# Performance work log

Measured on AMD Instinct MI355X. Metric: run time of the kernel, lower is better.

The kernel has to match this reference:

```python
import jax, jax.numpy as jnp
import numpy as np

B = 4096
ED = 128          # EMBEDDING_DIM
HD = 64           # HIDDEN_DIM
LH = 128          # LSTM_HIDDEN_DIM
IN_DIM = ED * (12 + 48 + 1)  # 7808
N_ABILITY, N_MOVE = 300, 900


def setup_inputs() -> dict:
    key = jax.random.key(0)
    ks = jax.random.split(key, 16)
    s = lambda k, shape, scale=0.05: (jax.random.normal(k, shape, dtype=jnp.float32) * scale)
    return {
        "ability_ids": jax.random.randint(ks[0], (B, 12), 0, N_ABILITY),
        "move_ids": jax.random.randint(ks[1], (B, 48), 0, N_MOVE),
        "numerical": s(ks[2], (B, 84), 1.0),
        "mask": (jax.random.uniform(ks[3], (B, 9)) > 0.3).astype(jnp.float32),
        "h0": jnp.zeros((B, LH), jnp.float32),
        "c0": jnp.zeros((B, LH), jnp.float32),
        "ability_emb": s(ks[4], (N_ABILITY, ED), 1.0),
        "move_emb": s(ks[5], (N_MOVE, ED), 1.0),
        "num_W": s(ks[6], (ED, 84)),
        "num_b": s(ks[7], (ED,)),
        "Wih": s(ks[8], (4 * LH, IN_DIM), 0.01),
        "Whh": s(ks[9], (4 * LH, LH)),
        "bih": s(ks[10], (4 * LH,)),
        "bhh": s(ks[11], (4 * LH,)),
        "W1": s(ks[12], (HD, LH)),
        "b1": s(ks[13], (HD,)),
        "W2": s(ks[14], (ED, HD)),
        "b2": s(ks[15], (ED,)),
        "Wa": s(jax.random.fold_in(key, 100), (9, ED)),
        "ba": s(jax.random.fold_in(key, 101), (9,)),
    }


def reference(ability_ids, move_ids, numerical, mask, h0, c0,
              ability_emb, move_emb, num_W, num_b,
              Wih, Whh, bih, bhh, W1, b1, W2, b2, Wa, ba):
    # Gather + concat: [B, 12*ED] + [B, 48*ED] + [B, ED] -> [B, 7808]
    ab = ability_emb[ability_ids].reshape(ability_ids.shape[0], 12 * ED)
    mv = move_emb[move_ids].reshape(move_ids.shape[0], 48 * ED)
    num = numerical @ num_W.T + num_b
    x = jnp.concatenate([ab, mv, num], axis=-1)

    # Single-timestep LSTM (torch gate order: i, f, g, o)
    gates = x @ Wih.T + bih + h0 @ Whh.T + bhh
    i, f, g, o = jnp.split(gates, 4, axis=-1)
    i, f, o = jax.nn.sigmoid(i), jax.nn.sigmoid(f), jax.nn.sigmoid(o)
    g = jnp.tanh(g)
    c1 = f * c0 + i * g
    h1 = o * jnp.tanh(c1)

    # MLP head + action logits
    feat = jax.nn.relu(h1 @ W1.T + b1) @ W2.T + b2
    probs = jax.nn.softmax(feat @ Wa.T + ba, axis=-1)

    # Masked renormalization; fall back to unmasked probs when mask kills everything
    masked = probs * mask
    ssum = masked.sum(-1, keepdims=True)
    out = jnp.where(ssum > 0, masked / jnp.where(ssum > 0, ssum, 1.0), probs)
    return out, h1, c1
```

## Files before the change

kernel.cpp:

```cpp
#include <hip/hip_runtime.h>
#include <hip/hip_bf16.h>
#include <stdint.h>
#include <stddef.h>

typedef __bf16 bf16;
typedef __bf16 bf16x4 __attribute__((ext_vector_type(4)));
typedef __bf16 bf16x8 __attribute__((ext_vector_type(8)));
typedef float f32x4 __attribute__((ext_vector_type(4)));

#define BATCH 4096
#define KIH 7808
#define KTOT 7936
#define NG 512
#define LH 128
#define HD 64
#define ED 128
#define SPLITK 4

#define OFF_WCAT 0u
#define OFF_GPART 8126464u
#define OFF_XT   24903680u
#define OFF_AB   27000832u
#define OFF_MV   27077632u
#define OFF_ADDR 27308032u
#define OFF_W1F  29405184u
#define OFF_W2F  29421568u
#define OFF_WAF  29437952u
#define OFF_NB   29442048u

#define O_H1 (BATCH * 9)
#define O_C1 (BATCH * 9 + BATCH * LH)

#define PREP_BP 2048
#define PREP_CW (PREP_BP + 512)
#define PREP_CE (PREP_CW + 150)
#define PREP_TOT (PREP_CE + 1)

typedef const __attribute__((address_space(1))) uint32_t* gas_ptr;
typedef __attribute__((address_space(3))) uint32_t* las_ptr;

__device__ __forceinline__ void async16(const void* g, void* l) {
    __builtin_amdgcn_global_load_lds((gas_ptr)g, (las_ptr)l, 16, 0, 0);
}

__global__ void prep(const int* __restrict__ ab_ids,
                     const int* __restrict__ mv_ids,
                     const float* __restrict__ numerical,
                     const float* __restrict__ h0,
                     const float* __restrict__ numW,
                     const float* __restrict__ numb,
                     const float* __restrict__ Wih,
                     const float* __restrict__ Whh,
                     const float* __restrict__ ab_emb,
                     const float* __restrict__ mv_emb,
                     const float* __restrict__ W1,
                     const float* __restrict__ W2,
                     const float* __restrict__ Wa,
                     uint8_t* __restrict__ ws) {
    const int bid = blockIdx.x;
    const int t = threadIdx.x;

    if (bid < PREP_BP) {
        bf16* xtail = (bf16*)(ws + OFF_XT);
        uint32_t* addrs = (uint32_t*)(ws + OFF_ADDR);
        const int h = t >> 7;
        const int th = t & 127;
        const int b = bid * 2 + h;

        __shared__ int ids[2][60];
        if (th < 60)
            ids[h][th] = (th < 12) ? ab_ids[b * 12 + th]
                                   : mv_ids[b * 48 + (th - 12)];

        const float v = (th < 84) ? numerical[(size_t)b * 84 + th] : 0.f;
        xtail[(size_t)b * 256 + th] = (bf16)v;
        xtail[(size_t)b * 256 + 128 + th] = (bf16)h0[(size_t)b * LH + th];
        __syncthreads();

        if (th < 64) {
            uint32_t off;
            if (th < 12) off = OFF_AB + (uint32_t)ids[h][th] * 256u;
            else if (th < 60) off = OFF_MV + (uint32_t)ids[h][th] * 256u;
            else if (th == 60) off = OFF_XT + (uint32_t)b * 512u;
            else if (th == 61) off = OFF_XT + (uint32_t)b * 512u + 256u;
            else off = OFF_XT;
            addrs[(size_t)b * 64 + th] = off;
        }
    } else if (bid < PREP_CW) {
        bf16* Wcat = (bf16*)(ws + OFF_WCAT);
        float* nbias = (float*)(ws + OFF_NB);
        const int n = bid - PREP_BP;

        __shared__ float wrow[128];
        __shared__ float nbs[128];
        if (t < 128) wrow[t] = Wih[(size_t)n * KIH + 7680 + t];
        else nbs[t - 128] = numb[t - 128];
        __syncthreads();

        const float* src_ih = Wih + (size_t)n * KIH;
        bf16* dst = Wcat + (size_t)n * KTOT;
        for (int k4 = t; k4 < 1920; k4 += 256) {
            const int k = k4 * 4;
            const float4 v = *(const float4*)(src_ih + k);
            bf16x4 o = {(bf16)v.x, (bf16)v.y, (bf16)v.z, (bf16)v.w};
            *(bf16x4*)(dst + k) = o;
        }
        if (t < 84) {
            float acc = 0.f;
#pragma unroll 4
            for (int e = 0; e < 128; ++e)
                acc += wrow[e] * numW[e * 84 + t];
            dst[7680 + t] = (bf16)acc;
        } else if (t < 128) {
            dst[7680 + t] = (bf16)0.f;
        } else {
            const int tt = t - 128;
            dst[KIH + tt] = (bf16)Whh[(size_t)n * LH + tt];
        }
        if (t == 255) {
            float a = 0.f;
#pragma unroll 4
            for (int e = 0; e < 128; ++e) a += wrow[e] * nbs[e];
            nbias[n] = a;
        }
    } else if (bid < PREP_CE) {
        bf16* ab8 = (bf16*)(ws + OFF_AB);
        bf16* mv8 = (bf16*)(ws + OFF_MV);
        const int i = ((bid - PREP_CW) * 256 + t) * 4;
        const bool isab = i < 300 * 128;
        const float4 v = isab ? *(const float4*)(ab_emb + i)
                              : *(const float4*)(mv_emb + (i - 300 * 128));
        bf16x4 o = {(bf16)v.x, (bf16)v.y, (bf16)v.z, (bf16)v.w};
        if (isab) *(bf16x4*)(ab8 + i) = o;
        else *(bf16x4*)(mv8 + (i - 300 * 128)) = o;
    } else {
        bf16* W1f = (bf16*)(ws + OFF_W1F);
        bf16* W2f = (bf16*)(ws + OFF_W2F);
        bf16* Waf = (bf16*)(ws + OFF_WAF);
        for (int e = t; e < 8192; e += 256) {
            const int j = e & 7, ln = (e >> 3) & 63, fid = e >> 9;
            const int kt = fid & 3, nt = fid >> 2;
            const int n = nt * 16 + (ln & 15);
            const int k = kt * 32 + (ln >> 4) * 8 + j;
            W1f[e] = (bf16)W1[n * 128 + k];
        }
        for (int e = t; e < 8192; e += 256) {
            const int j = e & 7, ln = (e >> 3) & 63, fid = e >> 9;
            const int kt = fid & 1, nt = fid >> 1;
            const int n = nt * 16 + (ln & 15);
            const int k = kt * 32 + (ln >> 4) * 8 + j;
            W2f[e] = (bf16)W2[n * 64 + k];
        }
        for (int e = t; e < 2048; e += 256) {
            const int j = e & 7, ln = (e >> 3) & 63, kt = e >> 9;
            const int n = ln & 15;
            const int k = kt * 32 + (ln >> 4) * 8 + j;
            Waf[e] = (n < 9) ? (bf16)Wa[n * 128 + k] : (bf16)0.f;
        }
    }
}

__global__ __launch_bounds__(256, 3) void gemm_gates(
    const uint8_t* __restrict__ wsbase,
    const bf16* __restrict__ Wcat,
    const uint32_t* __restrict__ addrs,
    bf16* __restrict__ gpart) {
    __shared__ bf16 As[2][64 * 64];
    __shared__ bf16 Bs[2][128 * 64];
    __shared__ uint32_t adr[17][64];

    const int tid = threadIdx.x;
    const int w = tid >> 6;
    const int lane = tid & 63;
    const int bm = blockIdx.x;
    const int bn = blockIdx.y;
    const int bz = blockIdx.z;
    const int kt_beg = bz * 31;
    const int kt_end = kt_beg + 31;

    const int s0 = kt_beg >> 1;
    const int ns = ((kt_end - 1) >> 1) - s0 + 1;
    for (int i = tid; i < ns * 64; i += 256) {
        adr[i >> 6][i & 63] =
            addrs[(size_t)(bm * 64 + (i & 63)) * 64 + s0 + (i >> 6)];
    }

    const int r_l = lane >> 3;
    const int sc16 = ((lane & 7) ^ r_l) * 16;

    const int wn = w & 1;
    const int wk = w >> 1;
    const int n0 = wn * 64;
    const int kk8 = wk * 4 + (lane >> 4);
    const int fl = lane & 15;

    f32x4 acc[4][4];
#pragma unroll
    for (int i = 0; i < 4; ++i)
#pragma unroll
        for (int j = 0; j < 4; ++j)
#pragma unroll
            for (int r = 0; r < 4; ++r) acc[i][j][r] = 0.f;

    __syncthreads();

    auto stage = [&](int kt, int pb) {
        const int k0 = kt * 64;
        const int sl = (kt >> 1) - s0;
        const int hb = (kt & 1) * 128;
#pragma unroll
        for (int j = 0; j < 2; ++j) {
            const int row = (w * 2 + j) * 8 + r_l;
            const uint8_t* gsrc = wsbase + adr[sl][row] + hb + sc16;
            async16(gsrc, (void*)&As[pb][((w * 2 + j) * 64 + lane) * 8]);
        }
#pragma unroll
        for (int j = 0; j < 4; ++j) {
            const int row = (w * 4 + j) * 8 + r_l;
            const bf16* gsrc = Wcat + (size_t)(bn * 128 + row) * KTOT + k0 + (sc16 >> 1);
            async16(gsrc, (void*)&Bs[pb][((w * 4 + j) * 64 + lane) * 8]);
        }
    };

    stage(kt_beg, 0);

    for (int kt = kt_beg; kt < kt_end; ++kt) {
        const int pb = (kt - kt_beg) & 1;
        __syncthreads();
        if (kt + 1 < kt_end) stage(kt + 1, pb ^ 1);

        const bf16* Ab = &As[pb][0];
        const bf16* Bb = &Bs[pb][0];

        bf16x8 bfr[4];
#pragma unroll
        for (int tj = 0; tj < 4; ++tj) {
            const int n = n0 + tj * 16 + fl;
            bfr[tj] = *(const bf16x8*)&Bb[n * 64 + ((kk8 ^ (n & 7)) * 8)];
        }
#pragma unroll
        for (int ti = 0; ti < 4; ++ti) {
            const int m = ti * 16 + fl;
            const bf16x8 af = *(const bf16x8*)&Ab[m * 64 + ((kk8 ^ (m & 7)) * 8)];
#pragma unroll
            for (int tj = 0; tj < 4; ++tj)
                acc[ti][tj] = __builtin_amdgcn_mfma_f32_16x16x32_bf16(
                    af, bfr[tj], acc[ti][tj], 0, 0, 0);
        }
    }

    __syncthreads();
    float* red = (wn == 0) ? (float*)&As[0][0] : (float*)&Bs[0][0];
    if (wk == 1) {
#pragma unroll
        for (int ti = 0; ti < 4; ++ti)
#pragma unroll
            for (int tj = 0; tj < 4; ++tj)
#pragma unroll
                for (int r = 0; r < 4; ++r)
                    red[((ti * 4 + tj) * 4 + r) * 64 + lane] = acc[ti][tj][r];
    }
    __syncthreads();

    if (wk == 0) {
        bf16* gdst = gpart + (size_t)bz * BATCH * NG;
        const int mlo = (lane >> 4) * 4;
#pragma unroll
        for (int ti = 0; ti < 4; ++ti)
#pragma unroll
            for (int tj = 0; tj < 4; ++tj) {
                const int mg = bm * 64 + ti * 16 + mlo;
                const int ng = bn * 128 + n0 + tj * 16 + fl;
                bf16* dst = gdst + (size_t)mg * NG + ng;
#pragma unroll
                for (int r = 0; r < 4; ++r)
                    dst[(size_t)r * NG] = (bf16)(
                        acc[ti][tj][r] + red[((ti * 4 + tj) * 4 + r) * 64 + lane]);
            }
    }
}

__global__ __launch_bounds__(256) void tail(
    const bf16* __restrict__ gpart,
    const float* __restrict__ bih, const float* __restrict__ bhh,
    const float* __restrict__ nbias, const float* __restrict__ c0,
    const float* __restrict__ mask,
    const bf16* __restrict__ W1f, const bf16* __restrict__ W2f,
    const bf16* __restrict__ Waf,
    const float* __restrict__ b1, const float* __restrict__ b2,
    const float* __restrict__ ba,
    float* __restrict__ out) {
    __shared__ bf16 hS[16 * 128];
    __shared__ bf16 uS[16 * 64];
    __shared__ bf16 fS[16 * 128];

    const int t = threadIdx.x;
    const int bid = blockIdx.x;
    const int b0 = bid * 16;

    {
        const int r = t >> 4;
        const int uc = (t & 15) * 8;
        const int b = b0 + r;

        float gv[4][8];
#pragma unroll
        for (int q = 0; q < 4; ++q)
#pragma unroll
            for (int hh = 0; hh < 2; ++hh) {
                const f32x4 va = *(const f32x4*)(bih + q * 128 + uc + hh * 4);
                const f32x4 vb = *(const f32x4*)(bhh + q * 128 + uc + hh * 4);
                const f32x4 vn = *(const f32x4*)(nbias + q * 128 + uc + hh * 4);
#pragma unroll
                for (int j = 0; j < 4; ++j)
                    gv[q][hh * 4 + j] = va[j] + vb[j] + vn[j];
            }
#pragma unroll
        for (int z = 0; z < SPLITK; ++z) {
            const bf16* gz = gpart + ((size_t)z * BATCH + b) * NG;
#pragma unroll
            for (int q = 0; q < 4; ++q) {
                const bf16x8 v = *(const bf16x8*)(gz + q * 128 + uc);
#pragma unroll
                for (int j = 0; j < 8; ++j) gv[q][j] += (float)v[j];
            }
        }

        const f32x4 c0a = *(const f32x4*)(c0 + (size_t)b * LH + uc);
        const f32x4 c0b = *(const f32x4*)(c0 + (size_t)b * LH + uc + 4);
        float h1v[8], c1v[8];
        bf16x8 hv8;
#pragma unroll
        for (int j = 0; j < 8; ++j) {
            const float iv = 1.f / (1.f + __expf(-gv[0][j]));
            const float fv = 1.f / (1.f + __expf(-gv[1][j]));
            const float gg = tanhf(gv[2][j]);
            const float ov = 1.f / (1.f + __expf(-gv[3][j]));
            const float c0j = (j < 4) ? c0a[j] : c0b[j - 4];
            const float c1 = fv * c0j + iv * gg;
            const float h1 = ov * tanhf(c1);
            c1v[j] = c1;
            h1v[j] = h1;
            hv8[j] = (bf16)h1;
        }
        *(bf16x8*)&hS[r * 128 + uc] = hv8;
        *(f32x4*)(out + O_H1 + (size_t)b * LH + uc) = *(const f32x4*)&h1v[0];
        *(f32x4*)(out + O_H1 + (size_t)b * LH + uc + 4) = *(const f32x4*)&h1v[4];
        *(f32x4*)(out + O_C1 + (size_t)b * LH + uc) = *(const f32x4*)&c1v[0];
        *(f32x4*)(out + O_C1 + (size_t)b * LH + uc + 4) = *(const f32x4*)&c1v[4];
    }
    __syncthreads();

    const int nl = t & 15, kg = (t & 63) >> 4;

    if (t < 64) {
        bf16x8 ah[4];
#pragma unroll
        for (int kt = 0; kt < 4; ++kt)
            ah[kt] = *(const bf16x8*)&hS[nl * 128 + kt * 32 + kg * 8];
#pragma unroll
        for (int nt = 0; nt < 4; ++nt) {
            f32x4 a = {0.f, 0.f, 0.f, 0.f};
#pragma unroll
            for (int kt = 0; kt < 4; ++kt)
                a = __builtin_amdgcn_mfma_f32_16x16x32_bf16(
                    ah[kt], *(const bf16x8*)&W1f[((nt * 4 + kt) * 64 + t) * 8],
                    a, 0, 0, 0);
            const int n = nt * 16 + nl;
            const float bb = b1[n];
#pragma unroll
            for (int rr = 0; rr < 4; ++rr)
                uS[(kg * 4 + rr) * 64 + n] = (bf16)fmaxf(a[rr] + bb, 0.f);
        }
    }
    __syncthreads();

    if (t < 64) {
        bf16x8 au[2];
#pragma unroll
        for (int kt = 0; kt < 2; ++kt)
            au[kt] = *(const bf16x8*)&uS[nl * 64 + kt * 32 + kg * 8];
#pragma unroll
        for (int nt = 0; nt < 8; ++nt) {
            f32x4 a = {0.f, 0.f, 0.f, 0.f};
#pragma unroll
            for (int kt = 0; kt < 2; ++kt)
                a = __builtin_amdgcn_mfma_f32_16x16x32_bf16(
                    au[kt], *(const bf16x8*)&W2f[((nt * 2 + kt) * 64 + t) * 8],
                    a, 0, 0, 0);
            const int n = nt * 16 + nl;
            const float bb = b2[n];
#pragma unroll
            for (int rr = 0; rr < 4; ++rr)
                fS[(kg * 4 + rr) * 128 + n] = (bf16)(a[rr] + bb);
        }
    }
    __syncthreads();

    if (t < 64) {
        bf16x8 afr[4];
#pragma unroll
        for (int kt = 0; kt < 4; ++kt)
            afr[kt] = *(const bf16x8*)&fS[nl * 128 + kt * 32 + kg * 8];

        f32x4 lg4 = {0.f, 0.f, 0.f, 0.f};
#pragma unroll
        for (int kt = 0; kt < 4; ++kt)
            lg4 = __builtin_amdgcn_mfma_f32_16x16x32_bf16(
                afr[kt], *(const bf16x8*)&Waf[(kt * 64 + t) * 8], lg4, 0, 0, 0);

        const float bav = (nl < 9) ? ba[nl] : 0.f;

#pragma unroll
        for (int rr = 0; rr < 4; ++rr) {
            const int b = b0 + kg * 4 + rr;
            float lg = (nl < 9) ? lg4[rr] + bav : -1e30f;
            float mx = lg;
#pragma unroll
            for (int off = 1; off < 16; off <<= 1)
                mx = fmaxf(mx, __shfl_xor(mx, off, 64));
            const float e = (nl < 9) ? __expf(lg - mx) : 0.f;
            const float mv = (nl < 9) ? mask[(size_t)b * 9 + nl] : 0.f;
            float tot = e, ms = e * mv;
#pragma unroll
            for (int off = 1; off < 16; off <<= 1) {
                tot += __shfl_xor(tot, off, 64);
                ms += __shfl_xor(ms, off, 64);
            }
            if (nl < 9)
                out[(size_t)b * 9 + nl] = (ms > 0.f) ? e * mv / ms : e / tot;
        }
    }
}

extern "C" void kernel_launch(void* const* d_in, const int* in_sizes, int n_in,
                              void* d_out, int out_size, void* d_ws, size_t ws_size,
                              hipStream_t stream) {
    const int* ab_ids = (const int*)d_in[0];
    const int* mv_ids = (const int*)d_in[1];
    const float* numerical = (const float*)d_in[2];
    const float* mask = (const float*)d_in[3];
    const float* h0 = (const float*)d_in[4];
    const float* c0 = (const float*)d_in[5];
    const float* ab_emb = (const float*)d_in[6];
    const float* mv_emb = (const float*)d_in[7];
    const float* numW = (const float*)d_in[8];
    const float* numb = (const float*)d_in[9];
    const float* Wih = (const float*)d_in[10];
    const float* Whh = (const float*)d_in[11];
    const float* bih = (const float*)d_in[12];
    const float* bhh = (const float*)d_in[13];
    const float* W1 = (const float*)d_in[14];
    const float* b1 = (const float*)d_in[15];
    const float* W2 = (const float*)d_in[16];
    const float* b2 = (const float*)d_in[17];
    const float* Wa = (const float*)d_in[18];
    const float* ba = (const float*)d_in[19];
    float* out = (float*)d_out;

    uint8_t* ws = (uint8_t*)d_ws;
    bf16* Wcat = (bf16*)(ws + OFF_WCAT);
    bf16* gpart = (bf16*)(ws + OFF_GPART);
    uint32_t* addrs = (uint32_t*)(ws + OFF_ADDR);
    bf16* W1f = (bf16*)(ws + OFF_W1F);
    bf16* W2f = (bf16*)(ws + OFF_W2F);
    bf16* Waf = (bf16*)(ws + OFF_WAF);
    float* nbias = (float*)(ws + OFF_NB);

    prep<<<PREP_TOT, 256, 0, stream>>>(
        ab_ids, mv_ids, numerical, h0, numW, numb, Wih, Whh, ab_emb, mv_emb,
        W1, W2, Wa, ws);
    gemm_gates<<<dim3(64, 4, 4), 256, 0, stream>>>(ws, Wcat, addrs, gpart);
    tail<<<BATCH / 16, 256, 0, stream>>>(gpart, bih, bhh, nbias, c0, mask,
                                         W1f, W2f, Waf, b1, b2, ba, out);
}
```

Before: 183.4 us.

## Retile gates GEMM to 128x128 tiles with 4-stage async pipeline

The gates GEMM moves from 64x128 tiles with an intra-block K split and an LDS reduction to 128x128 tiles with BK=32 and a 2x2 warp layout. A four-buffer LDS ring keeps two stages in flight, managed by explicit vmcnt waits and raw s_barriers. The cross-warp reduction goes away and each staged byte is reused across twice as many rows. In exchange the grid halves to 512 blocks, occupancy drops to two blocks per CU, and the manual waitcnt scheme is fragile.

```diff
diff --git a/kernel.cpp b/kernel.cpp
--- a/kernel.cpp
+++ b/kernel.cpp
@@ -160,14 +160,14 @@
     }
 }
 
-__global__ __launch_bounds__(256, 3) void gemm_gates(
+__global__ __launch_bounds__(256, 2) void gemm_gates(
     const uint8_t* __restrict__ wsbase,
     const bf16* __restrict__ Wcat,
     const uint32_t* __restrict__ addrs,
     bf16* __restrict__ gpart) {
-    __shared__ bf16 As[2][64 * 64];
-    __shared__ bf16 Bs[2][128 * 64];
-    __shared__ uint32_t adr[17][64];
+    __shared__ bf16 As[4][128 * 32];
+    __shared__ bf16 Bs[4][128 * 32];
+    __shared__ uint32_t adr[16][128];
 
     const int tid = threadIdx.x;
     const int w = tid >> 6;
@@ -175,25 +175,25 @@
     const int bm = blockIdx.x;
     const int bn = blockIdx.y;
     const int bz = blockIdx.z;
-    const int kt_beg = bz * 31;
-    const int kt_end = kt_beg + 31;
-
-    const int s0 = kt_beg >> 1;
-    const int ns = ((kt_end - 1) >> 1) - s0 + 1;
-    for (int i = tid; i < ns * 64; i += 256) {
-        adr[i >> 6][i & 63] =
-            addrs[(size_t)(bm * 64 + (i & 63)) * 64 + s0 + (i >> 6)];
-    }
-
-    const int r_l = lane >> 3;
-    const int sc16 = ((lane & 7) ^ r_l) * 16;
-
+
+    const int NS = 62;
+    const int kt_beg = bz * NS;
+
+    const int s0 = kt_beg >> 2;
+    const int ns = ((kt_beg + NS - 1) >> 2) - s0 + 1;
+    for (int i = tid; i < ns * 128; i += 256) {
+        adr[i >> 7][i & 127] =
+            addrs[(size_t)(bm * 128 + (i & 127)) * 64 + s0 + (i >> 7)];
+    }
+
+    const int wm = w >> 1;
     const int wn = w & 1;
-    const int wk = w >> 1;
-    const int n0 = wn * 64;
-    const int kk8 = wk * 4 + (lane >> 4);
+    const int kg = lane >> 4;
     const int fl = lane & 15;
 
+    const int rl = lane >> 2;
+    const int csw = (lane & 3) ^ (rl & 3);
+
     f32x4 acc[4][4];
 #pragma unroll
     for (int i = 0; i < 4; ++i)
@@ -204,80 +204,83 @@
 
     __syncthreads();
 
-    auto stage = [&](int kt, int pb) {
-        const int k0 = kt * 64;
-        const int sl = (kt >> 1) - s0;
-        const int hb = (kt & 1) * 128;
+    auto stage = [&](int i, int pb) {
+        const int kt = kt_beg + i;
+        const int sl = (kt >> 2) - s0;
+        const int qoff = (kt & 3) * 64;
+        const int k0 = kt * 32;
 #pragma unroll
         for (int j = 0; j < 2; ++j) {
-            const int row = (w * 2 + j) * 8 + r_l;
-            const uint8_t* gsrc = wsbase + adr[sl][row] + hb + sc16;
-            async16(gsrc, (void*)&As[pb][((w * 2 + j) * 64 + lane) * 8]);
-        }
-#pragma unroll
-        for (int j = 0; j < 4; ++j) {
-            const int row = (w * 4 + j) * 8 + r_l;
-            const bf16* gsrc = Wcat + (size_t)(bn * 128 + row) * KTOT + k0 + (sc16 >> 1);
-            async16(gsrc, (void*)&Bs[pb][((w * 4 + j) * 64 + lane) * 8]);
+            const int row = (w * 2 + j) * 16 + rl;
+            const uint8_t* ga = wsbase + adr[sl][row] + qoff + csw * 16;
+            async16(ga, (void*)&As[pb][(row * 4 + (lane & 3)) * 8]);
+        }
+#pragma unroll
+        for (int j = 0; j < 2; ++j) {
+            const int row = (w * 2 + j) * 16 + rl;
+            const bf16* gb =
+                Wcat + (size_t)(bn * 128 + row) * KTOT + k0 + csw * 8;
+            async16(gb, (void*)&Bs[pb][(row * 4 + (lane & 3)) * 8]);
         }
     };
 
-    stage(kt_beg, 0);
-
-    for (int kt = kt_beg; kt < kt_end; ++kt) {
-        const int pb = (kt - kt_beg) & 1;
-        __syncthreads();
-        if (kt + 1 < kt_end) stage(kt + 1, pb ^ 1);
-
+    auto compute = [&](int pb) {
         const bf16* Ab = &As[pb][0];
         const bf16* Bb = &Bs[pb][0];
-
-        bf16x8 bfr[4];
+        bf16x8 bfr[4], afr[4];
 #pragma unroll
         for (int tj = 0; tj < 4; ++tj) {
-            const int n = n0 + tj * 16 + fl;
-            bfr[tj] = *(const bf16x8*)&Bb[n * 64 + ((kk8 ^ (n & 7)) * 8)];
+            const int n = wn * 64 + tj * 16 + fl;
+            bfr[tj] = *(const bf16x8*)&Bb[n * 32 + ((kg ^ (n & 3)) * 8)];
         }
 #pragma unroll
         for (int ti = 0; ti < 4; ++ti) {
-            const int m = ti * 16 + fl;
-            const bf16x8 af = *(const bf16x8*)&Ab[m * 64 + ((kk8 ^ (m & 7)) * 8)];
+            const int m = wm * 64 + ti * 16 + fl;
+            afr[ti] = *(const bf16x8*)&Ab[m * 32 + ((kg ^ (m & 3)) * 8)];
+        }
+#pragma unroll
+        for (int ti = 0; ti < 4; ++ti)
 #pragma unroll
             for (int tj = 0; tj < 4; ++tj)
                 acc[ti][tj] = __builtin_amdgcn_mfma_f32_16x16x32_bf16(
-                    af, bfr[tj], acc[ti][tj], 0, 0, 0);
-        }
-    }
-
-    __syncthreads();
-    float* red = (wn == 0) ? (float*)&As[0][0] : (float*)&Bs[0][0];
-    if (wk == 1) {
-#pragma unroll
-        for (int ti = 0; ti < 4; ++ti)
-#pragma unroll
-            for (int tj = 0; tj < 4; ++tj)
-#pragma unroll
-                for (int r = 0; r < 4; ++r)
-                    red[((ti * 4 + tj) * 4 + r) * 64 + lane] = acc[ti][tj][r];
-    }
-    __syncthreads();
-
-    if (wk == 0) {
-        bf16* gdst = gpart + (size_t)bz * BATCH * NG;
-        const int mlo = (lane >> 4) * 4;
-#pragma unroll
-        for (int ti = 0; ti < 4; ++ti)
-#pragma unroll
-            for (int tj = 0; tj < 4; ++tj) {
-                const int mg = bm * 64 + ti * 16 + mlo;
-                const int ng = bn * 128 + n0 + tj * 16 + fl;
-                bf16* dst = gdst + (size_t)mg * NG + ng;
-#pragma unroll
-                for (int r = 0; r < 4; ++r)
-                    dst[(size_t)r * NG] = (bf16)(
-                        acc[ti][tj][r] + red[((ti * 4 + tj) * 4 + r) * 64 + lane]);
-            }
-    }
+                    afr[ti], bfr[tj], acc[ti][tj], 0, 0, 0);
+    };
+
+    stage(0, 0);
+    stage(1, 1);
+
+    for (int i = 0; i < NS - 2; ++i) {
+        stage(i + 2, (i + 2) & 3);
+        asm volatile("s_waitcnt vmcnt(8)" ::: "memory");
+        __builtin_amdgcn_sched_barrier(0);
+        __builtin_amdgcn_s_barrier();
+        compute(i & 3);
+    }
+    {
+        asm volatile("s_waitcnt vmcnt(4)" ::: "memory");
+        __builtin_amdgcn_sched_barrier(0);
+        __builtin_amdgcn_s_barrier();
+        compute((NS - 2) & 3);
+
+        asm volatile("s_waitcnt vmcnt(0)" ::: "memory");
+        __builtin_amdgcn_sched_barrier(0);
+        __builtin_amdgcn_s_barrier();
+        compute((NS - 1) & 3);
+    }
+
+    bf16* gdst = gpart + (size_t)bz * BATCH * NG;
+    const int mlo = (lane >> 4) * 4;
+#pragma unroll
+    for (int ti = 0; ti < 4; ++ti)
+#pragma unroll
+        for (int tj = 0; tj < 4; ++tj) {
+            const int mg = bm * 128 + wm * 64 + ti * 16 + mlo;
+            const int ng = bn * 128 + wn * 64 + tj * 16 + fl;
+            bf16* dst = gdst + (size_t)mg * NG + ng;
+#pragma unroll
+            for (int r = 0; r < 4; ++r)
+                dst[(size_t)r * NG] = (bf16)acc[ti][tj][r];
+        }
 }
 
 __global__ __launch_bounds__(256) void tail(
@@ -470,7 +473,7 @@
     prep<<<PREP_TOT, 256, 0, stream>>>(
         ab_ids, mv_ids, numerical, h0, numW, numb, Wih, Whh, ab_emb, mv_emb,
         W1, W2, Wa, ws);
-    gemm_gates<<<dim3(64, 4, 4), 256, 0, stream>>>(ws, Wcat, addrs, gpart);
+    gemm_gates<<<dim3(32, 4, 4), 256, 0, stream>>>(ws, Wcat, addrs, gpart);
     tail<<<BATCH / 16, 256, 0, stream>>>(gpart, bih, bhh, nbias, c0, mask,
                                          W1f, W2f, Waf, b1, b2, ba, out);
 }
```

Result: faster. 170.7 us (-6.9%).
